# Optimization experiments

Measured on AMD Instinct MI355X. Metric: run time of the kernel, lower is better.

## Reference

```python
import jax, jax.numpy as jnp
import numpy as np
import math

B = 2
D = 256
NH, NL, NP = 8, 4, 4
DH = D // NH
DFF = 1024
NLAYERS = 6
SHAPES = [(96, 96), (48, 48), (24, 24), (12, 12)]
CINS = [256, 512, 768, 1024]
LQ = sum(h * w for h, w in SHAPES)


def setup_inputs() -> dict:
    key = jax.random.key(0)
    ks = iter(jax.random.split(key, 64))
    inp = {}
    for i, (cin, (h, w)) in enumerate(zip(CINS, SHAPES)):
        inp[f"x{i+1}"] = jax.random.normal(next(ks), (B, cin, h, w), jnp.float32)
        inp[f"fc{i+1}_w"] = jax.random.normal(next(ks), (D, cin), jnp.float32) / np.sqrt(cin)
        inp[f"fc{i+1}_b"] = jnp.zeros((D,), jnp.float32)
    inp["gn_g"] = jnp.ones((4, D), jnp.float32)
    inp["gn_b"] = jnp.zeros((4, D), jnp.float32)
    inp["level_embed"] = jax.random.normal(next(ks), (4, D), jnp.float32)
    def lin(k, o, i_, s=1.0):
        return jax.random.normal(k, (NLAYERS, o, i_), jnp.float32) * (s / np.sqrt(i_))
    inp["off_w"] = lin(next(ks), NH * NL * NP * 2, D, 0.01)  # small, like zero-init offsets
    inp["off_b"] = jax.random.normal(next(ks), (NLAYERS, NH * NL * NP * 2), jnp.float32) * 0.5
    inp["aw_w"] = lin(next(ks), NH * NL * NP, D)
    inp["aw_b"] = jnp.zeros((NLAYERS, NH * NL * NP), jnp.float32)
    inp["val_w"] = lin(next(ks), D, D)
    inp["val_b"] = jnp.zeros((NLAYERS, D), jnp.float32)
    inp["out_w"] = lin(next(ks), D, D)
    inp["out_b"] = jnp.zeros((NLAYERS, D), jnp.float32)
    inp["ln1_g"] = jnp.ones((NLAYERS, D), jnp.float32)
    inp["ln1_b"] = jnp.zeros((NLAYERS, D), jnp.float32)
    inp["l1_w"] = lin(next(ks), DFF, D)
    inp["l1_b"] = jnp.zeros((NLAYERS, DFF), jnp.float32)
    inp["l2_w"] = lin(next(ks), D, DFF)
    inp["l2_b"] = jnp.zeros((NLAYERS, D), jnp.float32)
    inp["ln2_g"] = jnp.ones((NLAYERS, D), jnp.float32)
    inp["ln2_b"] = jnp.zeros((NLAYERS, D), jnp.float32)
    return inp


def layer_norm(x, g, b, eps=1e-5):
    m = x.mean(-1, keepdims=True)
    v = ((x - m) ** 2).mean(-1, keepdims=True)
    return (x - m) / jnp.sqrt(v + eps) * g + b


def group_norm(x, g, b, groups=32, eps=1e-5):
    # x: [B, L, C]; torch GroupNorm applied on [B, C, L] -> normalize over (group-channels, L)
    Bq, L, C = x.shape
    xg = x.reshape(Bq, L, groups, C // groups)
    m = xg.mean(axis=(1, 3), keepdims=True)
    v = ((xg - m) ** 2).mean(axis=(1, 3), keepdims=True)
    xg = (xg - m) / jnp.sqrt(v + eps)
    return xg.reshape(Bq, L, C) * g + b


def sine_pos(Hl, Wl):
    # DETR PositionEmbeddingSine, normalize=True, mask all-zero -> cumsum = arange(1..)
    eps, scale, T, npf = 1e-6, 2 * math.pi, 10000.0, D // 2
    ye = (jnp.arange(1, Hl + 1, dtype=jnp.float32) / (Hl + eps)) * scale
    xe = (jnp.arange(1, Wl + 1, dtype=jnp.float32) / (Wl + eps)) * scale
    dim_t = T ** (2 * (jnp.arange(npf) // 2).astype(jnp.float32) / npf)
    def emb(e):
        p = e[:, None] / dim_t
        return jnp.stack([jnp.sin(p[:, 0::2]), jnp.cos(p[:, 1::2])], -1).reshape(-1, npf)
    py, px = emb(ye), emb(xe)
    pos = jnp.concatenate([
        jnp.broadcast_to(py[:, None, :], (Hl, Wl, npf)),
        jnp.broadcast_to(px[None, :, :], (Hl, Wl, npf))], -1)
    return pos.reshape(Hl * Wl, D)


def ref_points():
    # training path: all levels, valid_ratios == 1 (masks all zero)
    refs = []
    for (Hl, Wl) in SHAPES:
        ry = (jnp.arange(Hl, dtype=jnp.float32) + 0.5) / Hl
        rx = (jnp.arange(Wl, dtype=jnp.float32) + 0.5) / Wl
        gy, gx = jnp.meshgrid(ry, rx, indexing='ij')
        refs.append(jnp.stack([gx.ravel(), gy.ravel()], -1))
    r = jnp.concatenate(refs, 0)  # [LQ, 2]
    return jnp.broadcast_to(r[None, :, None, :], (B, LQ, NL, 2))


def ms_deform(value, locs, attw):
    # value: [B, Lin, NH, DH]; locs: [B, Lq, NH, NL, NP, 2] in [0,1]; attw: [B, Lq, NH, NL, NP]
    Bq, Lq = locs.shape[0], locs.shape[1]
    out = jnp.zeros((Bq, Lq, NH, DH), value.dtype)
    start = 0
    for l, (Hl, Wl) in enumerate(SHAPES):
        vf = value[:, start:start + Hl * Wl].transpose(0, 2, 1, 3)  # [B, NH, HW, DH]
        start += Hl * Wl
        loc = locs[:, :, :, l]  # [B, Lq, NH, NP, 2]
        # grid_sample align_corners=False unnormalize: (2u-1+1)/2*W - 0.5 = u*W - 0.5
        x = loc[..., 0] * Wl - 0.5
        y = loc[..., 1] * Hl - 0.5
        x0, y0 = jnp.floor(x), jnp.floor(y)
        tx, ty = x - x0, y - y0
        samp = jnp.zeros((Bq, NH, Lq * NP, DH), value.dtype)
        for dx, dy, w in ((0, 0, (1 - tx) * (1 - ty)), (1, 0, tx * (1 - ty)),
                          (0, 1, (1 - tx) * ty), (1, 1, tx * ty)):
            xi, yi = x0 + dx, y0 + dy
            valid = (xi >= 0) & (xi < Wl) & (yi >= 0) & (yi < Hl)  # zero padding
            idx = (jnp.clip(yi, 0, Hl - 1) * Wl + jnp.clip(xi, 0, Wl - 1)).astype(jnp.int32)
            idxr = idx.transpose(0, 2, 1, 3).reshape(Bq, NH, Lq * NP)
            g = jnp.take_along_axis(vf, idxr[..., None], axis=2)  # [B, NH, Lq*NP, DH]
            wr = (w * valid).transpose(0, 2, 1, 3).reshape(Bq, NH, Lq * NP, 1)
            samp = samp + g * wr
        samp = samp.reshape(Bq, NH, Lq, NP, DH)
        out = out + jnp.einsum('bnqpd,bqnp->bqnd', samp, attw[:, :, :, l])
    return out.reshape(Bq, Lq, NH * DH)


def enc_layer(src, pos, ref, p):
    q = src + pos
    Bq, Lq, _ = src.shape
    off = (q @ p['off_w'].T + p['off_b']).reshape(Bq, Lq, NH, NL, NP, 2)
    aw = jax.nn.softmax((q @ p['aw_w'].T + p['aw_b']).reshape(Bq, Lq, NH, NL * NP), -1)
    aw = aw.reshape(Bq, Lq, NH, NL, NP)
    val = (src @ p['val_w'].T + p['val_b']).reshape(Bq, Lq, NH, DH)
    norml = jnp.array([[w, h] for (h, w) in SHAPES], jnp.float32)  # [NL, 2] as (W, H)
    locs = ref[:, :, None, :, None, :] + off / norml[None, None, None, :, None, :]
    att = ms_deform(val, locs, aw) @ p['out_w'].T + p['out_b']
    src = layer_norm(src + att, p['ln1_g'], p['ln1_b'])
    h = jax.nn.relu(src @ p['l1_w'].T + p['l1_b'])
    src = layer_norm(src + h @ p['l2_w'].T + p['l2_b'], p['ln2_g'], p['ln2_b'])
    return src


LAYER_KEYS = ['off_w', 'off_b', 'aw_w', 'aw_b', 'val_w', 'val_b', 'out_w', 'out_b',
              'ln1_g', 'ln1_b', 'l1_w', 'l1_b', 'l2_w', 'l2_b', 'ln2_g', 'ln2_b']


def _forward(x1, x2, x3, x4, fcs, gn_g, gn_b, level_embed, stacks):
    xs = [x1, x2, x3, x4]
    toks, poss = [], []
    for i, x in enumerate(xs):
        Bq, c, h, w = x.shape
        f = x.reshape(Bq, c, h * w).transpose(0, 2, 1)  # b (h w) c
        t = group_norm(f @ fcs[i][0].T + fcs[i][1], gn_g[i], gn_b[i])
        toks.append(t)
        poss.append(jnp.broadcast_to((sine_pos(h, w) + level_embed[i])[None], (Bq, h * w, D)))
    src = jnp.concatenate(toks, 1)
    pos = jnp.concatenate(poss, 1)
    ref = ref_points()
    for l in range(NLAYERS):
        p = {k: stacks[k][l] for k in LAYER_KEYS}
        src = enc_layer(src, pos, ref, p)
    return src


def reference(x1, x2, x3, x4, fc1_w, fc1_b, fc2_w, fc2_b, fc3_w, fc3_b, fc4_w, fc4_b,
              gn_g, gn_b, level_embed, off_w, off_b, aw_w, aw_b, val_w, val_b, out_w, out_b,
              ln1_g, ln1_b, l1_w, l1_b, l2_w, l2_b, ln2_g, ln2_b):
    fcs = [(fc1_w, fc1_b), (fc2_w, fc2_b), (fc3_w, fc3_b), (fc4_w, fc4_b)]
    stacks = dict(off_w=off_w, off_b=off_b, aw_w=aw_w, aw_b=aw_b, val_w=val_w, val_b=val_b,
                  out_w=out_w, out_b=out_b, ln1_g=ln1_g, ln1_b=ln1_b, l1_w=l1_w, l1_b=l1_b,
                  l2_w=l2_w, l2_b=l2_b, ln2_g=ln2_g, ln2_b=ln2_b)
    src = _forward(x1, x2, x3, x4, fcs, gn_g, gn_b, level_embed, stacks)
    spatial_shapes = jnp.array(SHAPES, jnp.int32)
    level_start_index = jnp.concatenate([jnp.zeros((1,), jnp.int32),
                                         jnp.cumsum(spatial_shapes.prod(1))[:-1]])
    valid_ratios = jnp.ones((B, NL, 2), jnp.float32)
    return (src, level_start_index, spatial_shapes, valid_ratios)
```

## Files before the change

### kernel.cpp

```cpp
#include <hip/hip_runtime.h>
#include <math.h>

#define DD 256
#define DFFN 1024
#define LQT 12240
#define BB 2
#define MROWS (BB * LQT)

typedef __attribute__((ext_vector_type(8))) short short8v;
typedef __attribute__((ext_vector_type(4))) float floatx4;

__device__ __forceinline__ unsigned short f2bf(float x) {
    unsigned int u = __builtin_bit_cast(unsigned int, x);
    u = (u + 0x7fffu + ((u >> 16) & 1u)) >> 16;
    return (unsigned short)u;
}
__device__ __forceinline__ float bf2f(unsigned short h) {
    unsigned int u = ((unsigned int)h) << 16;
    return __builtin_bit_cast(float, u);
}

__device__ __forceinline__ void gload16(const unsigned short* g, unsigned short* lds) {
    __builtin_amdgcn_global_load_lds(
        (const __attribute__((address_space(1))) unsigned int*)g,
        (__attribute__((address_space(3))) unsigned int*)lds, 16, 0, 0);
}

__device__ __forceinline__ void level_of(int q, int& lvl, int& start, int& S) {
    if (q < 9216)       { lvl = 0; start = 0;     S = 96; }
    else if (q < 11520) { lvl = 1; start = 9216;  S = 48; }
    else if (q < 12096) { lvl = 2; start = 11520; S = 24; }
    else                { lvl = 3; start = 12096; S = 12; }
}

__global__ __launch_bounds__(256)
void gemm_qkv(const unsigned short* __restrict__ Aq,
              const unsigned short* __restrict__ Asr,
              const unsigned short* __restrict__ Woff,
              const unsigned short* __restrict__ Waw,
              const unsigned short* __restrict__ Wval,
              const float* __restrict__ boff, const float* __restrict__ baw,
              const float* __restrict__ bval,
              float* __restrict__ awbo, unsigned short* __restrict__ offo,
              unsigned short* __restrict__ valo)
{
    __shared__ alignas(16) unsigned short As[2][4][64][8];
    __shared__ alignas(16) unsigned short Bs[2][4][128][8];
    const int t = threadIdx.x;
    const int m0 = blockIdx.x * 64;
    const int y = blockIdx.y;
    const unsigned short* A; const unsigned short* Wb; const float* bi;
    int nb, mode;
    if (y < 3) {
        A = Aq;
        if (y < 2) { Wb = Woff; bi = boff; nb = y * 128; mode = 0; }
        else       { Wb = Waw;  bi = baw;  nb = 0;       mode = 1; }
    } else {
        A = Asr; Wb = Wval; bi = bval; nb = (y - 3) * 128; mode = 2;
    }
    const int wv = __builtin_amdgcn_readfirstlane(t >> 6);
    const int lane = t & 63;
    const int wm = wv >> 1, wn = wv & 1;
    const int kb = lane >> 4, lr = lane & 15;

    const int ar = min(m0 + lane, MROWS - 1);
    const unsigned short* gA  = A  + (long)ar * 256 + wv * 8;
    const unsigned short* gB0 = Wb + (long)(nb + lane) * 256 + wv * 8;
    const unsigned short* gB1 = Wb + (long)(nb + 64 + lane) * 256 + wv * 8;

    floatx4 acc[2][4];
    #pragma unroll
    for (int m = 0; m < 2; ++m)
        #pragma unroll
        for (int n = 0; n < 4; ++n)
            acc[m][n] = (floatx4){0.f, 0.f, 0.f, 0.f};

    gload16(gA,  &As[0][wv][0][0]);
    gload16(gB0, &Bs[0][wv][0][0]);
    gload16(gB1, &Bs[0][wv][64][0]);
    gA += 32; gB0 += 32; gB1 += 32;
    __syncthreads();

    #pragma unroll
    for (int kt = 0; kt < 8; ++kt) {
        const int cur = kt & 1;
        if (kt < 7) {
            gload16(gA,  &As[cur ^ 1][wv][0][0]);
            gload16(gB0, &Bs[cur ^ 1][wv][0][0]);
            gload16(gB1, &Bs[cur ^ 1][wv][64][0]);
            gA += 32; gB0 += 32; gB1 += 32;
        }
        short8v av[2], bv[4];
        #pragma unroll
        for (int m = 0; m < 2; ++m)
            av[m] = *(const short8v*)&As[cur][kb][wm * 32 + m * 16 + lr][0];
        #pragma unroll
        for (int n = 0; n < 4; ++n)
            bv[n] = *(const short8v*)&Bs[cur][kb][wn * 64 + n * 16 + lr][0];
        #pragma unroll
        for (int m = 0; m < 2; ++m)
            #pragma unroll
            for (int n = 0; n < 4; ++n)
                acc[m][n] = __builtin_amdgcn_mfma_f32_16x16x32_bf16(
                    av[m], bv[n], acc[m][n], 0, 0, 0);
        __syncthreads();
    }

    const int lh = lane >> 4;
    #pragma unroll
    for (int m = 0; m < 2; ++m) {
        const int row0 = m0 + wm * 32 + m * 16 + lh * 4;
        #pragma unroll
        for (int n = 0; n < 4; ++n) {
            const int col = nb + wn * 64 + n * 16 + lr;
            const float b = bi[col];
            #pragma unroll
            for (int r = 0; r < 4; ++r) {
                const int row = row0 + r;
                if (row >= MROWS) continue;
                const float v = acc[m][n][r] + b;
                if (mode == 0)      offo[(long)row * 256 + col] = f2bf(v);
                else if (mode == 1) awbo[(long)row * 128 + col] = v;
                else                valo[(long)row * 256 + col] = f2bf(v);
            }
        }
    }
}

__global__ __launch_bounds__(256)
void gemm64(const unsigned short* __restrict__ A, long aZ,
            const unsigned short* __restrict__ W,
            const float* __restrict__ bias,
            float* __restrict__ Cf, long cZ,
            int M, int N, int K)
{
    __shared__ alignas(16) unsigned short As[2][4][64][8];
    __shared__ alignas(16) unsigned short Bs[2][4][128][8];
    const int t = threadIdx.x;
    const int z = blockIdx.z;
    A  += (long)z * aZ;
    Cf += (long)z * cZ;
    const int m0 = blockIdx.x * 64;
    const int n0 = blockIdx.y * 128;
    const int wv = __builtin_amdgcn_readfirstlane(t >> 6);
    const int lane = t & 63;
    const int wm = wv >> 1, wn = wv & 1;
    const int kb = lane >> 4, lr = lane & 15;

    const int ar = min(m0 + lane, M - 1);
    const unsigned short* gA  = A + (long)ar * K + wv * 8;
    const unsigned short* gB0 = W + (long)(n0 + lane) * K + wv * 8;
    const unsigned short* gB1 = W + (long)(n0 + 64 + lane) * K + wv * 8;

    floatx4 acc[2][4];
    #pragma unroll
    for (int m = 0; m < 2; ++m)
        #pragma unroll
        for (int n = 0; n < 4; ++n)
            acc[m][n] = (floatx4){0.f, 0.f, 0.f, 0.f};

    gload16(gA,  &As[0][wv][0][0]);
    gload16(gB0, &Bs[0][wv][0][0]);
    gload16(gB1, &Bs[0][wv][64][0]);
    gA += 32; gB0 += 32; gB1 += 32;
    __syncthreads();

    const int nk = K >> 5;
    for (int kt = 0; kt < nk; ++kt) {
        const int cur = kt & 1;
        if (kt + 1 < nk) {
            gload16(gA,  &As[cur ^ 1][wv][0][0]);
            gload16(gB0, &Bs[cur ^ 1][wv][0][0]);
            gload16(gB1, &Bs[cur ^ 1][wv][64][0]);
            gA += 32; gB0 += 32; gB1 += 32;
        }
        short8v av[2], bv[4];
        #pragma unroll
        for (int m = 0; m < 2; ++m)
            av[m] = *(const short8v*)&As[cur][kb][wm * 32 + m * 16 + lr][0];
        #pragma unroll
        for (int n = 0; n < 4; ++n)
            bv[n] = *(const short8v*)&Bs[cur][kb][wn * 64 + n * 16 + lr][0];
        #pragma unroll
        for (int m = 0; m < 2; ++m)
            #pragma unroll
            for (int n = 0; n < 4; ++n)
                acc[m][n] = __builtin_amdgcn_mfma_f32_16x16x32_bf16(
                    av[m], bv[n], acc[m][n], 0, 0, 0);
        __syncthreads();
    }

    const int lh = lane >> 4;
    #pragma unroll
    for (int m = 0; m < 2; ++m) {
        const int row0 = m0 + wm * 32 + m * 16 + lh * 4;
        #pragma unroll
        for (int n = 0; n < 4; ++n) {
            const int col = n0 + wn * 64 + n * 16 + lr;
            const float b = bias[col];
            #pragma unroll
            for (int r = 0; r < 4; ++r) {
                const int row = row0 + r;
                if (row >= M) continue;
                Cf[(long)row * N + col] = acc[m][n][r] + b;
            }
        }
    }
}

__global__ __launch_bounds__(256)
void gemm128(const unsigned short* __restrict__ A,
             const unsigned short* __restrict__ W,
             const float* __restrict__ bias, unsigned short* __restrict__ Ch,
             int M, int N, int K)
{
    __shared__ alignas(16) unsigned short As[2][4][128][8];
    __shared__ alignas(16) unsigned short Bs[2][4][128][8];
    const int t = threadIdx.x;
    const int m0 = blockIdx.x * 128;
    const int n0 = blockIdx.y * 128;
    const int wv = __builtin_amdgcn_readfirstlane(t >> 6);
    const int lane = t & 63;
    const int wm = wv >> 1, wn = wv & 1;
    const int kb = lane >> 4, lr = lane & 15;

    const int r0 = min(m0 + lane, M - 1);
    const int r1 = min(m0 + 64 + lane, M - 1);
    const unsigned short* gA0 = A + (long)r0 * K + wv * 8;
    const unsigned short* gA1 = A + (long)r1 * K + wv * 8;
    const unsigned short* gB0 = W + (long)(n0 + lane) * K + wv * 8;
    const unsigned short* gB1 = W + (long)(n0 + 64 + lane) * K + wv * 8;

    floatx4 acc[4][4];
    #pragma unroll
    for (int m = 0; m < 4; ++m)
        #pragma unroll
        for (int n = 0; n < 4; ++n)
            acc[m][n] = (floatx4){0.f, 0.f, 0.f, 0.f};

    gload16(gA0, &As[0][wv][0][0]);
    gload16(gA1, &As[0][wv][64][0]);
    gload16(gB0, &Bs[0][wv][0][0]);
    gload16(gB1, &Bs[0][wv][64][0]);
    gA0 += 32; gA1 += 32; gB0 += 32; gB1 += 32;
    __syncthreads();

    const int nk = K >> 5;
    for (int kt = 0; kt < nk; ++kt) {
        const int cur = kt & 1;
        if (kt + 1 < nk) {
            gload16(gA0, &As[cur ^ 1][wv][0][0]);
            gload16(gA1, &As[cur ^ 1][wv][64][0]);
            gload16(gB0, &Bs[cur ^ 1][wv][0][0]);
            gload16(gB1, &Bs[cur ^ 1][wv][64][0]);
            gA0 += 32; gA1 += 32; gB0 += 32; gB1 += 32;
        }
        short8v av[4], bv[4];
        #pragma unroll
        for (int m = 0; m < 4; ++m)
            av[m] = *(const short8v*)&As[cur][kb][wm * 64 + m * 16 + lr][0];
        #pragma unroll
        for (int n = 0; n < 4; ++n)
            bv[n] = *(const short8v*)&Bs[cur][kb][wn * 64 + n * 16 + lr][0];
        #pragma unroll
        for (int m = 0; m < 4; ++m)
            #pragma unroll
            for (int n = 0; n < 4; ++n)
                acc[m][n] = __builtin_amdgcn_mfma_f32_16x16x32_bf16(
                    av[m], bv[n], acc[m][n], 0, 0, 0);
        __syncthreads();
    }

    const int lh = lane >> 4;
    #pragma unroll
    for (int m = 0; m < 4; ++m) {
        const int row0 = m0 + wm * 64 + m * 16 + lh * 4;
        #pragma unroll
        for (int n = 0; n < 4; ++n) {
            const int col = n0 + wn * 64 + n * 16 + lr;
            const float b = bias[col];
            #pragma unroll
            for (int r = 0; r < 4; ++r) {
                const int row = row0 + r;
                if (row >= M) continue;
                Ch[(long)row * N + col] = f2bf(fmaxf(acc[m][n][r] + b, 0.f));
            }
        }
    }
}

__global__ __launch_bounds__(256)
void gemm_ln(const unsigned short* __restrict__ A,
             const unsigned short* __restrict__ W,
             const float* __restrict__ bias, const unsigned short* R,
             const float* __restrict__ lg, const float* __restrict__ lb,
             float* outf, unsigned short* outh,
             const float* __restrict__ pos, unsigned short* __restrict__ qout,
             int M, int K)
{
    __shared__ alignas(16) unsigned short As[2][4][32][8];
    __shared__ alignas(16) unsigned short Bs[2][4][256][8];
    __shared__ float red[32][4][2];
    __shared__ float smean[32], sinv[32];
    const int t = threadIdx.x;
    const int m0 = blockIdx.x * 32;
    const int wv = __builtin_amdgcn_readfirstlane(t >> 6);
    const int lane = t & 63;
    const int kb = lane >> 4, lr = lane & 15;
    const int lh = kb;

    const unsigned short* gA = A + (long)(m0 + (lane & 31)) * K
                                 + (wv * 2 + (lane >> 5)) * 8;
    const unsigned short* gB0 = W + (long)lane * K + wv * 8;
    const unsigned short* gB1 = W + (long)(64 + lane) * K + wv * 8;
    const unsigned short* gB2 = W + (long)(128 + lane) * K + wv * 8;
    const unsigned short* gB3 = W + (long)(192 + lane) * K + wv * 8;

    floatx4 acc[2][4];
    #pragma unroll
    for (int m = 0; m < 2; ++m)
        #pragma unroll
        for (int n = 0; n < 4; ++n)
            acc[m][n] = (floatx4){0.f, 0.f, 0.f, 0.f};

    if (wv < 2) gload16(gA, &As[0][wv * 2][0][0]);
    gload16(gB0, &Bs[0][wv][0][0]);
    gload16(gB1, &Bs[0][wv][64][0]);
    gload16(gB2, &Bs[0][wv][128][0]);
    gload16(gB3, &Bs[0][wv][192][0]);
    gA += 32; gB0 += 32; gB1 += 32; gB2 += 32; gB3 += 32;
    __syncthreads();

    const int nk = K >> 5;
    for (int kt = 0; kt < nk; ++kt) {
        const int cur = kt & 1;
        if (kt + 1 < nk) {
            if (wv < 2) gload16(gA, &As[cur ^ 1][wv * 2][0][0]);
            gload16(gB0, &Bs[cur ^ 1][wv][0][0]);
            gload16(gB1, &Bs[cur ^ 1][wv][64][0]);
            gload16(gB2, &Bs[cur ^ 1][wv][128][0]);
            gload16(gB3, &Bs[cur ^ 1][wv][192][0]);
            gA += 32; gB0 += 32; gB1 += 32; gB2 += 32; gB3 += 32;
        }
        short8v av[2], bv[4];
        #pragma unroll
        for (int m = 0; m < 2; ++m)
            av[m] = *(const short8v*)&As[cur][kb][m * 16 + lr][0];
        #pragma unroll
        for (int n = 0; n < 4; ++n)
            bv[n] = *(const short8v*)&Bs[cur][kb][wv * 64 + n * 16 + lr][0];
        #pragma unroll
        for (int m = 0; m < 2; ++m)
            #pragma unroll
            for (int n = 0; n < 4; ++n)
                acc[m][n] = __builtin_amdgcn_mfma_f32_16x16x32_bf16(
                    av[m], bv[n], acc[m][n], 0, 0, 0);
        __syncthreads();
    }

    #pragma unroll
    for (int n = 0; n < 4; ++n) {
        const int col = wv * 64 + n * 16 + lr;
        const float bcol = bias[col];
        #pragma unroll
        for (int m = 0; m < 2; ++m) {
            #pragma unroll
            for (int r = 0; r < 4; ++r) {
                const int grow = m0 + m * 16 + lh * 4 + r;
                acc[m][n][r] += bcol + bf2f(R[(long)grow * 256 + col]);
            }
        }
    }
    #pragma unroll
    for (int m = 0; m < 2; ++m) {
        #pragma unroll
        for (int r = 0; r < 4; ++r) {
            float s = acc[m][0][r] + acc[m][1][r] + acc[m][2][r] + acc[m][3][r];
            float q = acc[m][0][r] * acc[m][0][r] + acc[m][1][r] * acc[m][1][r]
                    + acc[m][2][r] * acc[m][2][r] + acc[m][3][r] * acc[m][3][r];
            #pragma unroll
            for (int o = 1; o < 16; o <<= 1) {
                s += __shfl_xor(s, o);
                q += __shfl_xor(q, o);
            }
            if (lr == 0) {
                red[m * 16 + lh * 4 + r][wv][0] = s;
                red[m * 16 + lh * 4 + r][wv][1] = q;
            }
        }
    }
    __syncthreads();
    if (t < 32) {
        const float s = red[t][0][0] + red[t][1][0] + red[t][2][0] + red[t][3][0];
        const float q = red[t][0][1] + red[t][1][1] + red[t][2][1] + red[t][3][1];
        const float mean = s * (1.f / 256.f);
        smean[t] = mean;
        sinv[t] = rsqrtf(q * (1.f / 256.f) - mean * mean + 1e-5f);
    }
    __syncthreads();
    #pragma unroll
    for (int n = 0; n < 4; ++n) {
        const int col = wv * 64 + n * 16 + lr;
        const float gc = lg[col], bc = lb[col];
        #pragma unroll
        for (int m = 0; m < 2; ++m) {
            #pragma unroll
            for (int r = 0; r < 4; ++r) {
                const int row = m * 16 + lh * 4 + r;
                const int grow = m0 + row;
                const float y = (acc[m][n][r] - smean[row]) * sinv[row] * gc + bc;
                const long o = (long)grow * 256 + col;
                outh[o] = f2bf(y);
                if (outf) outf[o] = y;
                if (qout) {
                    const int qrow = grow - (grow >= LQT ? LQT : 0);
                    qout[o] = f2bf(y + pos[(long)qrow * 256 + col]);
                }
            }
        }
    }
}

__global__ __launch_bounds__(256)
void tp_k(const float* __restrict__ x, unsigned short* __restrict__ xt,
          int C, int Ml)
{
    __shared__ float tile[32][33];
    const int m0 = blockIdx.x * 32, c0 = blockIdx.y * 32;
    const int zb = blockIdx.z;
    const float* px = x + (long)zb * C * Ml;
    unsigned short* pxt = xt + (long)zb * Ml * C;
    const int t = threadIdx.x;
    {
        const int cl = t >> 3, m4 = (t & 7) * 4;
        const int gm = m0 + m4;
        if (gm < Ml) {
            const float4 v = *(const float4*)(px + (long)(c0 + cl) * Ml + gm);
            tile[cl][m4 + 0] = v.x; tile[cl][m4 + 1] = v.y;
            tile[cl][m4 + 2] = v.z; tile[cl][m4 + 3] = v.w;
        }
    }
    __syncthreads();
    {
        const int ml = t >> 3, c4 = (t & 7) * 4;
        const int gm = m0 + ml;
        if (gm < Ml) {
            ushort4 o;
            o.x = f2bf(tile[c4 + 0][ml]);
            o.y = f2bf(tile[c4 + 1][ml]);
            o.z = f2bf(tile[c4 + 2][ml]);
            o.w = f2bf(tile[c4 + 3][ml]);
            *(ushort4*)(pxt + (long)gm * C + c0 + c4) = o;
        }
    }
}

__global__ __launch_bounds__(256)
void gn_part(const float* __restrict__ src, float* __restrict__ part)
{
    const int x = blockIdx.x;
    const int b = x >> 7, c = x & 127;
    int lvl, chunk;
    if (c < 96)       { lvl = 0; chunk = c; }
    else if (c < 120) { lvl = 1; chunk = c - 96; }
    else if (c < 126) { lvl = 2; chunk = c - 120; }
    else              { lvl = 3; chunk = c - 126; }
    const int starts[4] = {0, 9216, 11520, 12096};
    const int crows[4]  = {96, 96, 96, 72};
    const int rows = crows[lvl];
    const long base = ((long)b * LQT + starts[lvl] + (long)chunk * rows) * DD;
    const int t = threadIdx.x;
    float s = 0.f, sq = 0.f;
    for (int r = 0; r < rows; ++r) {
        const float v = src[base + (long)r * DD + t];
        s += v; sq += v * v;
    }
    #pragma unroll
    for (int o = 1; o < 8; o <<= 1) {
        s  += __shfl_xor(s, o);
        sq += __shfl_xor(sq, o);
    }
    if ((t & 7) == 0) {
        float* p = part + ((long)x * 32 + (t >> 3)) * 2;
        p[0] = s; p[1] = sq;
    }
}

__global__ void gn_fin(const float* __restrict__ part, float* __restrict__ stat)
{
    const int t = threadIdx.x;
    const int b = t >> 7, rest = t & 127;
    const int lvl = rest >> 5, grp = rest & 31;
    const int cbase[4] = {0, 96, 120, 126};
    const int ccnt[4]  = {96, 24, 6, 2};
    const int Ml[4]    = {9216, 2304, 576, 144};
    float s = 0.f, sq = 0.f;
    for (int i = 0; i < ccnt[lvl]; ++i) {
        const float* p = part + ((long)(b * 128 + cbase[lvl] + i) * 32 + grp) * 2;
        s += p[0]; sq += p[1];
    }
// ... 195 lines not shown
                              hipStream_t stream)
{
    const float* xs[4]  = {(const float*)d_in[0], (const float*)d_in[3],
                           (const float*)d_in[6], (const float*)d_in[9]};
    const float* fcw[4] = {(const float*)d_in[1], (const float*)d_in[4],
                           (const float*)d_in[7], (const float*)d_in[10]};
    const float* fcb[4] = {(const float*)d_in[2], (const float*)d_in[5],
                           (const float*)d_in[8], (const float*)d_in[11]};
    const float* gn_g = (const float*)d_in[12];
    const float* gn_b = (const float*)d_in[13];
    const float* lemb = (const float*)d_in[14];
    const float* off_w = (const float*)d_in[15];
    const float* off_b = (const float*)d_in[16];
    const float* aw_w  = (const float*)d_in[17];
    const float* aw_b  = (const float*)d_in[18];
    const float* val_w = (const float*)d_in[19];
    const float* val_b = (const float*)d_in[20];
    const float* out_w = (const float*)d_in[21];
    const float* out_b = (const float*)d_in[22];
    const float* ln1_g = (const float*)d_in[23];
    const float* ln1_b = (const float*)d_in[24];
    const float* l1_w  = (const float*)d_in[25];
    const float* l1_b  = (const float*)d_in[26];
    const float* l2_w  = (const float*)d_in[27];
    const float* l2_b  = (const float*)d_in[28];
    const float* ln2_g = (const float*)d_in[29];
    const float* ln2_b = (const float*)d_in[30];

    float* src = (float*)d_out;
    float* ws = (float*)d_ws;
    float* pos = ws;
    float* awb = pos + 3133440;
    unsigned short* bigbuf = (unsigned short*)(awb + 3133440);
    unsigned short* xt     = bigbuf;
    unsigned short* off_bf = bigbuf;
    unsigned short* val_bf = bigbuf + 6266880;
    unsigned short* msd_bf = bigbuf + 12533760;
    unsigned short* hid_bf = bigbuf;
    unsigned short* q_bf   = bigbuf + 25067520;
    unsigned short* src_bf = q_bf + 6266880;
    unsigned short* wb     = src_bf + 6266880;
    unsigned short* wb_fc[4];
    wb_fc[0] = wb;
    wb_fc[1] = wb_fc[0] + 65536;
    wb_fc[2] = wb_fc[1] + 131072;
    wb_fc[3] = wb_fc[2] + 196608;
    unsigned short* wb_off = wb_fc[3] + 262144;
    unsigned short* wb_aw  = wb_off + 393216;
    unsigned short* wb_val = wb_aw  + 196608;
    unsigned short* wb_out = wb_val + 393216;
    unsigned short* wb_l1  = wb_out + 393216;
    unsigned short* wb_l2  = wb_l1  + 1572864;
    float* part = (float*)(wb_l2 + 1572864);
    float* stat = part + 16384;
    (void)in_sizes; (void)n_in; (void)out_size; (void)ws_size;

    const int CINS[4]   = {256, 512, 768, 1024};
    const int SS[4]     = {96, 48, 24, 12};
    const int STARTS[4] = {0, 9216, 11520, 12096};
    const long XTOFF[4] = {0, 4718592, 7077888, 7962624};

    pos_k<<<LQT, 256, 0, stream>>>(pos, lemb);
    wcvt_k<<<(WCVT_TOTAL / 4 + 255) / 256, 256, 0, stream>>>(
        fcw[0], fcw[1], fcw[2], fcw[3], off_w, aw_w, val_w, out_w, l1_w, l2_w, wb);

    for (int i = 0; i < 4; ++i) {
        const int Ml = SS[i] * SS[i];
        tp_k<<<dim3((Ml + 31) / 32, CINS[i] / 32, BB), 256, 0, stream>>>(
            xs[i], xt + XTOFF[i], CINS[i], Ml);
    }
    for (int i = 0; i < 4; ++i) {
        const int Ml = SS[i] * SS[i];
        gemm64<<<dim3((Ml + 63) / 64, 2, BB), 256, 0, stream>>>(
            xt + XTOFF[i], (long)Ml * CINS[i],
            wb_fc[i], fcb[i],
            src + (long)STARTS[i] * DD, (long)LQT * DD,
            Ml, DD, CINS[i]);
    }
    gn_part<<<256, 256, 0, stream>>>(src, part);
    gn_fin<<<1, 256, 0, stream>>>(part, stat);
    gn_apply<<<MROWS / 4, 256, 0, stream>>>(src, src_bf, q_bf, stat, gn_g, gn_b, pos);

    for (int l = 0; l < 6; ++l) {
        gemm_qkv<<<dim3(383, 5), 256, 0, stream>>>(
            q_bf, src_bf,
            wb_off + (long)l * 65536, wb_aw + (long)l * 32768,
            wb_val + (long)l * 65536,
            off_b + l * DD, aw_b + l * 128, val_b + l * DD,
            awb, off_bf, val_bf);
        msdeform_k<<<MROWS / 2, 256, 0, stream>>>(val_bf, off_bf, awb, msd_bf);
        gemm_ln<<<765, 256, 0, stream>>>(
            msd_bf, wb_out + (long)l * 65536, out_b + l * DD, src_bf,
            ln1_g + l * DD, ln1_b + l * DD, nullptr, src_bf,
            nullptr, nullptr, MROWS, DD);
        gemm128<<<dim3(192, 8), 256, 0, stream>>>(
            src_bf, wb_l1 + (long)l * 262144, l1_b + l * DFFN, hid_bf,
            MROWS, DFFN, DD);
        const bool last = (l == 5);
        gemm_ln<<<765, 256, 0, stream>>>(
            hid_bf, wb_l2 + (long)l * 262144, l2_b + l * DD, src_bf,
            ln2_g + l * DD, ln2_b + l * DD, last ? src : nullptr, src_bf,
            last ? nullptr : pos, last ? nullptr : q_bf, MROWS, DFFN);
    }
    tail_k<<<1, 32, 0, stream>>>(src + (long)BB * LQT * DD);
}
```

Measured before the change: 1.593 ms.

## Stage whole A tile in LDS once and stream weights from global to registers

After: 1.731 ms. +8.7%, slower.

```diff
diff --git a/kernel.cpp b/kernel.cpp
--- a/kernel.cpp
+++ b/kernel.cpp
@@ -33,95 +33,255 @@
     else                { lvl = 3; start = 12096; S = 12; }
 }
 
-__global__ __launch_bounds__(256)
-void gemm_qkv(const unsigned short* __restrict__ Aq,
-              const unsigned short* __restrict__ Asr,
-              const unsigned short* __restrict__ Woff,
-              const unsigned short* __restrict__ Waw,
-              const unsigned short* __restrict__ Wval,
-              const float* __restrict__ boff, const float* __restrict__ baw,
-              const float* __restrict__ bval,
-              float* __restrict__ awbo, unsigned short* __restrict__ offo,
-              unsigned short* __restrict__ valo)
-{
-    __shared__ alignas(16) unsigned short As[2][4][64][8];
-    __shared__ alignas(16) unsigned short Bs[2][4][128][8];
-    const int t = threadIdx.x;
+template<int MF, int NF, int KO>
+__device__ __forceinline__ void as_core(const unsigned short* __restrict__ A,
+                                        const unsigned short* __restrict__ W,
+                                        unsigned short* AsD, int m0, int ncol0,
+                                        int M, floatx4 (&acc)[MF][NF])
+{
+    constexpr int BM = MF * 16;
+    constexpr int K  = KO * 32;
+    const int t = threadIdx.x;
+    const int wv = t >> 6, lane = t & 63;
+    const int lr = lane & 15;
+
+    constexpr int CH = BM * K / 512;
+    constexpr int PW = CH / 4;
+    #pragma unroll
+    for (int c = 0; c < PW; ++c) {
+        const int ch = wv * PW + c;
+        int row, sl;
+        if (BM == 64) { row = lane;      sl = ch; }
+        else          { row = lane & 31; sl = 2 * ch + (lane >> 5); }
+        gload16(A + (long)min(m0 + row, M - 1) * K + sl * 8, AsD + ch * 512);
+    }
+    __syncthreads();
+
+    const unsigned short* bp[NF];
+    #pragma unroll
+    for (int nf = 0; nf < NF; ++nf)
+        bp[nf] = W + (long)(ncol0 + nf * 16 + lr) * K + (lane >> 4) * 8;
+    const unsigned short* ap = AsD + (lane >> 4) * BM * 8 + lr * 8;
+
+    uint4 b0[NF], b1[NF];
+    short8v a0[MF], a1[MF];
+    #pragma unroll
+    for (int nf = 0; nf < NF; ++nf) b0[nf] = *(const uint4*)(bp[nf]);
+    #pragma unroll
+    for (int m = 0; m < MF; ++m)   a0[m] = *(const short8v*)(ap + m * 128);
+
+    for (int ko = 0; ko < KO; ko += 2) {
+        #pragma unroll
+        for (int nf = 0; nf < NF; ++nf)
+            b1[nf] = *(const uint4*)(bp[nf] + (ko + 1) * 32);
+        #pragma unroll
+        for (int m = 0; m < MF; ++m)
+            a1[m] = *(const short8v*)(ap + (long)(ko + 1) * BM * 32 + m * 128);
+        #pragma unroll
+        for (int m = 0; m < MF; ++m)
+            #pragma unroll
+            for (int nf = 0; nf < NF; ++nf)
+                acc[m][nf] = __builtin_amdgcn_mfma_f32_16x16x32_bf16(
+                    a0[m], __builtin_bit_cast(short8v, b0[nf]), acc[m][nf], 0, 0, 0);
+        if (ko + 2 < KO) {
+            #pragma unroll
+            for (int nf = 0; nf < NF; ++nf)
+                b0[nf] = *(const uint4*)(bp[nf] + (ko + 2) * 32);
+            #pragma unroll
+            for (int m = 0; m < MF; ++m)
+                a0[m] = *(const short8v*)(ap + (long)(ko + 2) * BM * 32 + m * 128);
+        }
+        #pragma unroll
+        for (int m = 0; m < MF; ++m)
+            #pragma unroll
+            for (int nf = 0; nf < NF; ++nf)
+                acc[m][nf] = __builtin_amdgcn_mfma_f32_16x16x32_bf16(
+                    a1[m], __builtin_bit_cast(short8v, b1[nf]), acc[m][nf], 0, 0, 0);
+    }
+}
+
+__global__ __launch_bounds__(256)
+void gemm_as_qkv(const unsigned short* __restrict__ Aq,
+                 const unsigned short* __restrict__ Asr,
+                 const unsigned short* __restrict__ Woff,
+                 const unsigned short* __restrict__ Waw,
+                 const unsigned short* __restrict__ Wval,
+                 const float* __restrict__ boff, const float* __restrict__ baw,
+                 const float* __restrict__ bval,
+                 float* __restrict__ awbo, unsigned short* __restrict__ offo,
+                 unsigned short* __restrict__ valo, int M)
+{
+    extern __shared__ __align__(16) unsigned short AsD[];
+    const int y = blockIdx.y;
     const int m0 = blockIdx.x * 64;
-    const int y = blockIdx.y;
-    const unsigned short* A; const unsigned short* Wb; const float* bi;
+    const unsigned short* A; const unsigned short* W; const float* bi;
     int nb, mode;
     if (y < 3) {
         A = Aq;
-        if (y < 2) { Wb = Woff; bi = boff; nb = y * 128; mode = 0; }
-        else       { Wb = Waw;  bi = baw;  nb = 0;       mode = 1; }
+        if (y < 2) { W = Woff; bi = boff; nb = y * 128; mode = 0; }
+        else       { W = Waw;  bi = baw;  nb = 0;       mode = 1; }
     } else {
-        A = Asr; Wb = Wval; bi = bval; nb = (y - 3) * 128; mode = 2;
-    }
-    const int wv = __builtin_amdgcn_readfirstlane(t >> 6);
-    const int lane = t & 63;
-    const int wm = wv >> 1, wn = wv & 1;
-    const int kb = lane >> 4, lr = lane & 15;
-
-    const int ar = min(m0 + lane, MROWS - 1);
-    const unsigned short* gA  = A  + (long)ar * 256 + wv * 8;
-    const unsigned short* gB0 = Wb + (long)(nb + lane) * 256 + wv * 8;
-    const unsigned short* gB1 = Wb + (long)(nb + 64 + lane) * 256 + wv * 8;
-
-    floatx4 acc[2][4];
-    #pragma unroll
-    for (int m = 0; m < 2; ++m)
-        #pragma unroll
-        for (int n = 0; n < 4; ++n)
+        A = Asr; W = Wval; bi = bval; nb = (y - 3) * 128; mode = 2;
+    }
+    const int t = threadIdx.x;
+    const int wv = t >> 6, lane = t & 63, lr = lane & 15, lh = lane >> 4;
+
+    floatx4 acc[4][2];
+    #pragma unroll
+    for (int m = 0; m < 4; ++m)
+        #pragma unroll
+        for (int n = 0; n < 2; ++n)
             acc[m][n] = (floatx4){0.f, 0.f, 0.f, 0.f};
 
-    gload16(gA,  &As[0][wv][0][0]);
-    gload16(gB0, &Bs[0][wv][0][0]);
-    gload16(gB1, &Bs[0][wv][64][0]);
-    gA += 32; gB0 += 32; gB1 += 32;
-    __syncthreads();
-
-    #pragma unroll
-    for (int kt = 0; kt < 8; ++kt) {
-        const int cur = kt & 1;
-        if (kt < 7) {
-            gload16(gA,  &As[cur ^ 1][wv][0][0]);
-            gload16(gB0, &Bs[cur ^ 1][wv][0][0]);
-            gload16(gB1, &Bs[cur ^ 1][wv][64][0]);
-            gA += 32; gB0 += 32; gB1 += 32;
-        }
-        short8v av[2], bv[4];
-        #pragma unroll
-        for (int m = 0; m < 2; ++m)
-            av[m] = *(const short8v*)&As[cur][kb][wm * 32 + m * 16 + lr][0];
-        #pragma unroll
-        for (int n = 0; n < 4; ++n)
-            bv[n] = *(const short8v*)&Bs[cur][kb][wn * 64 + n * 16 + lr][0];
-        #pragma unroll
-        for (int m = 0; m < 2; ++m)
-            #pragma unroll
-            for (int n = 0; n < 4; ++n)
-                acc[m][n] = __builtin_amdgcn_mfma_f32_16x16x32_bf16(
-                    av[m], bv[n], acc[m][n], 0, 0, 0);
-        __syncthreads();
-    }
-
-    const int lh = lane >> 4;
-    #pragma unroll
-    for (int m = 0; m < 2; ++m) {
-        const int row0 = m0 + wm * 32 + m * 16 + lh * 4;
-        #pragma unroll
-        for (int n = 0; n < 4; ++n) {
-            const int col = nb + wn * 64 + n * 16 + lr;
+    as_core<4, 2, 8>(A, W, AsD, m0, nb + wv * 32, M, acc);
+
+    #pragma unroll
+    for (int m = 0; m < 4; ++m) {
+        #pragma unroll
+        for (int nf = 0; nf < 2; ++nf) {
+            const int col = nb + wv * 32 + nf * 16 + lr;
             const float b = bi[col];
             #pragma unroll
             for (int r = 0; r < 4; ++r) {
-                const int row = row0 + r;
-                if (row >= MROWS) continue;
-                const float v = acc[m][n][r] + b;
+                const int row = m0 + m * 16 + lh * 4 + r;
+                if (row >= M) continue;
+                const float v = acc[m][nf][r] + b;
                 if (mode == 0)      offo[(long)row * 256 + col] = f2bf(v);
                 else if (mode == 1) awbo[(long)row * 128 + col] = v;
                 else                valo[(long)row * 256 + col] = f2bf(v);
+            }
+        }
+    }
+}
+
+__global__ __launch_bounds__(256)
+void gemm_as_relu(const unsigned short* __restrict__ A,
+                  const unsigned short* __restrict__ W,
+                  const float* __restrict__ bias,
+                  unsigned short* __restrict__ Ch, int M)
+{
+    extern __shared__ __align__(16) unsigned short AsD[];
+    const int m0 = blockIdx.x * 64;
+    const int n0 = blockIdx.y * 256;
+    const int t = threadIdx.x;
+    const int wv = t >> 6, lane = t & 63, lr = lane & 15, lh = lane >> 4;
+
+    floatx4 acc[4][4];
+    #pragma unroll
+    for (int m = 0; m < 4; ++m)
+        #pragma unroll
+        for (int n = 0; n < 4; ++n)
+            acc[m][n] = (floatx4){0.f, 0.f, 0.f, 0.f};
+
+    as_core<4, 4, 8>(A, W, AsD, m0, n0 + wv * 64, M, acc);
+
+    #pragma unroll
+    for (int m = 0; m < 4; ++m) {
+        #pragma unroll
+        for (int nf = 0; nf < 4; ++nf) {
+            const int col = n0 + wv * 64 + nf * 16 + lr;
+            const float b = bias[col];
+            #pragma unroll
+            for (int r = 0; r < 4; ++r) {
+                const int row = m0 + m * 16 + lh * 4 + r;
+                if (row >= M) continue;
+                Ch[(long)row * 1024 + col] = f2bf(fmaxf(acc[m][nf][r] + b, 0.f));
+            }
+        }
+    }
+}
+
+template<int MF, int KO>
+__global__ __launch_bounds__(256)
+void gemm_as_ln(const unsigned short* __restrict__ A,
+                const unsigned short* __restrict__ W,
+                const float* __restrict__ bias, const unsigned short* R,
+                const float* __restrict__ lg, const float* __restrict__ lb,
+                float* outf, unsigned short* outh,
+                const float* __restrict__ pos, unsigned short* __restrict__ qout,
+                int M)
+{
+    extern __shared__ __align__(16) unsigned short AsD[];
+    constexpr int BM = MF * 16;
+    const int m0 = blockIdx.x * BM;
+    const int t = threadIdx.x;
+    const int wv = t >> 6, lane = t & 63, lr = lane & 15, lh = lane >> 4;
+
+    floatx4 acc[MF][4];
+    #pragma unroll
+    for (int m = 0; m < MF; ++m)
+        #pragma unroll
+        for (int n = 0; n < 4; ++n)
+            acc[m][n] = (floatx4){0.f, 0.f, 0.f, 0.f};
+
+    as_core<MF, 4, KO>(A, W, AsD, m0, wv * 64, M, acc);
+
+    __syncthreads();
+    float* red   = (float*)AsD;
+    float* smean = red + BM * 8;
+    float* sinv  = smean + BM;
+
+    #pragma unroll
+    for (int nf = 0; nf < 4; ++nf) {
+        const int col = wv * 64 + nf * 16 + lr;
+        const float bcol = bias[col];
+        #pragma unroll
+        for (int m = 0; m < MF; ++m) {
+            #pragma unroll
+            for (int r = 0; r < 4; ++r) {
+                const int grow = m0 + m * 16 + lh * 4 + r;
+                const int rr = min(grow, M - 1);
+                acc[m][nf][r] += bcol + bf2f(R[(long)rr * 256 + col]);
+            }
+        }
+    }
+    #pragma unroll
+    for (int m = 0; m < MF; ++m) {
+        #pragma unroll
+        for (int r = 0; r < 4; ++r) {
+            float s = acc[m][0][r] + acc[m][1][r] + acc[m][2][r] + acc[m][3][r];
+            float q = acc[m][0][r] * acc[m][0][r] + acc[m][1][r] * acc[m][1][r]
+                    + acc[m][2][r] * acc[m][2][r] + acc[m][3][r] * acc[m][3][r];
+            #pragma unroll
+            for (int o = 1; o < 16; o <<= 1) {
+                s += __shfl_xor(s, o);
+                q += __shfl_xor(q, o);
+            }
+            if (lr == 0) {
+                const int row = m * 16 + lh * 4 + r;
+                red[row * 8 + wv * 2 + 0] = s;
+                red[row * 8 + wv * 2 + 1] = q;
+            }
+        }
+    }
+    __syncthreads();
+    if (t < BM) {
+        const float s = red[t * 8 + 0] + red[t * 8 + 2] + red[t * 8 + 4] + red[t * 8 + 6];
+        const float q = red[t * 8 + 1] + red[t * 8 + 3] + red[t * 8 + 5] + red[t * 8 + 7];
+        const float mean = s * (1.f / 256.f);
+        smean[t] = mean;
+        sinv[t] = rsqrtf(q * (1.f / 256.f) - mean * mean + 1e-5f);
+    }
+    __syncthreads();
+    #pragma unroll
+    for (int nf = 0; nf < 4; ++nf) {
+        const int col = wv * 64 + nf * 16 + lr;
+        const float gc = lg[col], bc = lb[col];
+        #pragma unroll
+        for (int m = 0; m < MF; ++m) {
+            #pragma unroll
+            for (int r = 0; r < 4; ++r) {
+                const int row = m * 16 + lh * 4 + r;
+                const int grow = m0 + row;
+                if (grow >= M) continue;
+                const float y = (acc[m][nf][r] - smean[row]) * sinv[row] * gc + bc;
+                const long o = (long)grow * 256 + col;
+                outh[o] = f2bf(y);
+                if (outf) outf[o] = y;
+                if (qout) {
+                    const int qrow = grow - (grow >= LQT ? LQT : 0);
+                    qout[o] = f2bf(y + pos[(long)qrow * 256 + col]);
+                }
             }
         }
     }
@@ -203,219 +363,6 @@
                 const int row = row0 + r;
                 if (row >= M) continue;
                 Cf[(long)row * N + col] = acc[m][n][r] + b;
-            }
-        }
-    }
-}
-
-__global__ __launch_bounds__(256)
-void gemm128(const unsigned short* __restrict__ A,
-             const unsigned short* __restrict__ W,
-             const float* __restrict__ bias, unsigned short* __restrict__ Ch,
-             int M, int N, int K)
-{
-    __shared__ alignas(16) unsigned short As[2][4][128][8];
-    __shared__ alignas(16) unsigned short Bs[2][4][128][8];
-    const int t = threadIdx.x;
-    const int m0 = blockIdx.x * 128;
-    const int n0 = blockIdx.y * 128;
-    const int wv = __builtin_amdgcn_readfirstlane(t >> 6);
-    const int lane = t & 63;
-    const int wm = wv >> 1, wn = wv & 1;
-    const int kb = lane >> 4, lr = lane & 15;
-
-    const int r0 = min(m0 + lane, M - 1);
-    const int r1 = min(m0 + 64 + lane, M - 1);
-    const unsigned short* gA0 = A + (long)r0 * K + wv * 8;
-    const unsigned short* gA1 = A + (long)r1 * K + wv * 8;
-    const unsigned short* gB0 = W + (long)(n0 + lane) * K + wv * 8;
-    const unsigned short* gB1 = W + (long)(n0 + 64 + lane) * K + wv * 8;
-
-    floatx4 acc[4][4];
-    #pragma unroll
-    for (int m = 0; m < 4; ++m)
-        #pragma unroll
-        for (int n = 0; n < 4; ++n)
-            acc[m][n] = (floatx4){0.f, 0.f, 0.f, 0.f};
-
-    gload16(gA0, &As[0][wv][0][0]);
-    gload16(gA1, &As[0][wv][64][0]);
-    gload16(gB0, &Bs[0][wv][0][0]);
-    gload16(gB1, &Bs[0][wv][64][0]);
-    gA0 += 32; gA1 += 32; gB0 += 32; gB1 += 32;
-    __syncthreads();
-
-    const int nk = K >> 5;
-    for (int kt = 0; kt < nk; ++kt) {
-        const int cur = kt & 1;
-        if (kt + 1 < nk) {
-            gload16(gA0, &As[cur ^ 1][wv][0][0]);
-            gload16(gA1, &As[cur ^ 1][wv][64][0]);
-            gload16(gB0, &Bs[cur ^ 1][wv][0][0]);
-            gload16(gB1, &Bs[cur ^ 1][wv][64][0]);
-            gA0 += 32; gA1 += 32; gB0 += 32; gB1 += 32;
-        }
-        short8v av[4], bv[4];
-        #pragma unroll
-        for (int m = 0; m < 4; ++m)
-            av[m] = *(const short8v*)&As[cur][kb][wm * 64 + m * 16 + lr][0];
-        #pragma unroll
-        for (int n = 0; n < 4; ++n)
-            bv[n] = *(const short8v*)&Bs[cur][kb][wn * 64 + n * 16 + lr][0];
-        #pragma unroll
-        for (int m = 0; m < 4; ++m)
-            #pragma unroll
-            for (int n = 0; n < 4; ++n)
-                acc[m][n] = __builtin_amdgcn_mfma_f32_16x16x32_bf16(
-                    av[m], bv[n], acc[m][n], 0, 0, 0);
-        __syncthreads();
-    }
-
-    const int lh = lane >> 4;
-    #pragma unroll
-    for (int m = 0; m < 4; ++m) {
-        const int row0 = m0 + wm * 64 + m * 16 + lh * 4;
-        #pragma unroll
-        for (int n = 0; n < 4; ++n) {
-            const int col = n0 + wn * 64 + n * 16 + lr;
-            const float b = bias[col];
-            #pragma unroll
-            for (int r = 0; r < 4; ++r) {
-                const int row = row0 + r;
-                if (row >= M) continue;
-                Ch[(long)row * N + col] = f2bf(fmaxf(acc[m][n][r] + b, 0.f));
-            }
-        }
-    }
-}
-
-__global__ __launch_bounds__(256)
-void gemm_ln(const unsigned short* __restrict__ A,
-             const unsigned short* __restrict__ W,
-             const float* __restrict__ bias, const unsigned short* R,
-             const float* __restrict__ lg, const float* __restrict__ lb,
-             float* outf, unsigned short* outh,
-             const float* __restrict__ pos, unsigned short* __restrict__ qout,
-             int M, int K)
-{
-    __shared__ alignas(16) unsigned short As[2][4][32][8];
-    __shared__ alignas(16) unsigned short Bs[2][4][256][8];
-    __shared__ float red[32][4][2];
-    __shared__ float smean[32], sinv[32];
-    const int t = threadIdx.x;
-    const int m0 = blockIdx.x * 32;
-    const int wv = __builtin_amdgcn_readfirstlane(t >> 6);
-    const int lane = t & 63;
-    const int kb = lane >> 4, lr = lane & 15;
-    const int lh = kb;
-
-    const unsigned short* gA = A + (long)(m0 + (lane & 31)) * K
-                                 + (wv * 2 + (lane >> 5)) * 8;
-    const unsigned short* gB0 = W + (long)lane * K + wv * 8;
-    const unsigned short* gB1 = W + (long)(64 + lane) * K + wv * 8;
-    const unsigned short* gB2 = W + (long)(128 + lane) * K + wv * 8;
-    const unsigned short* gB3 = W + (long)(192 + lane) * K + wv * 8;
-
-    floatx4 acc[2][4];
-    #pragma unroll
-    for (int m = 0; m < 2; ++m)
-        #pragma unroll
-        for (int n = 0; n < 4; ++n)
-            acc[m][n] = (floatx4){0.f, 0.f, 0.f, 0.f};
-
-    if (wv < 2) gload16(gA, &As[0][wv * 2][0][0]);
-    gload16(gB0, &Bs[0][wv][0][0]);
-    gload16(gB1, &Bs[0][wv][64][0]);
-    gload16(gB2, &Bs[0][wv][128][0]);
-    gload16(gB3, &Bs[0][wv][192][0]);
-    gA += 32; gB0 += 32; gB1 += 32; gB2 += 32; gB3 += 32;
-    __syncthreads();
-
-    const int nk = K >> 5;
-    for (int kt = 0; kt < nk; ++kt) {
-        const int cur = kt & 1;
-        if (kt + 1 < nk) {
-            if (wv < 2) gload16(gA, &As[cur ^ 1][wv * 2][0][0]);
-            gload16(gB0, &Bs[cur ^ 1][wv][0][0]);
-            gload16(gB1, &Bs[cur ^ 1][wv][64][0]);
-            gload16(gB2, &Bs[cur ^ 1][wv][128][0]);
-            gload16(gB3, &Bs[cur ^ 1][wv][192][0]);
-            gA += 32; gB0 += 32; gB1 += 32; gB2 += 32; gB3 += 32;
-        }
-        short8v av[2], bv[4];
-        #pragma unroll
-        for (int m = 0; m < 2; ++m)
-            av[m] = *(const short8v*)&As[cur][kb][m * 16 + lr][0];
-        #pragma unroll
-        for (int n = 0; n < 4; ++n)
-            bv[n] = *(const short8v*)&Bs[cur][kb][wv * 64 + n * 16 + lr][0];
-        #pragma unroll
-        for (int m = 0; m < 2; ++m)
-            #pragma unroll
-            for (int n = 0; n < 4; ++n)
-                acc[m][n] = __builtin_amdgcn_mfma_f32_16x16x32_bf16(
-                    av[m], bv[n], acc[m][n], 0, 0, 0);
-        __syncthreads();
-    }
-
-    #pragma unroll
-    for (int n = 0; n < 4; ++n) {
-        const int col = wv * 64 + n * 16 + lr;
-        const float bcol = bias[col];
-        #pragma unroll
-        for (int m = 0; m < 2; ++m) {
-            #pragma unroll
-            for (int r = 0; r < 4; ++r) {
-                const int grow = m0 + m * 16 + lh * 4 + r;
-                acc[m][n][r] += bcol + bf2f(R[(long)grow * 256 + col]);
-            }
-        }
-    }
-    #pragma unroll
-    for (int m = 0; m < 2; ++m) {
-        #pragma unroll
-        for (int r = 0; r < 4; ++r) {
-            float s = acc[m][0][r] + acc[m][1][r] + acc[m][2][r] + acc[m][3][r];
-            float q = acc[m][0][r] * acc[m][0][r] + acc[m][1][r] * acc[m][1][r]
-                    + acc[m][2][r] * acc[m][2][r] + acc[m][3][r] * acc[m][3][r];
-            #pragma unroll
-            for (int o = 1; o < 16; o <<= 1) {
-                s += __shfl_xor(s, o);
-                q += __shfl_xor(q, o);
-            }
-            if (lr == 0) {
-                red[m * 16 + lh * 4 + r][wv][0] = s;
-                red[m * 16 + lh * 4 + r][wv][1] = q;
-            }
-        }
-    }
-    __syncthreads();
-    if (t < 32) {
-        const float s = red[t][0][0] + red[t][1][0] + red[t][2][0] + red[t][3][0];
-        const float q = red[t][0][1] + red[t][1][1] + red[t][2][1] + red[t][3][1];
-        const float mean = s * (1.f / 256.f);
-        smean[t] = mean;
-        sinv[t] = rsqrtf(q * (1.f / 256.f) - mean * mean + 1e-5f);
-    }
-    __syncthreads();
-    #pragma unroll
-    for (int n = 0; n < 4; ++n) {
-        const int col = wv * 64 + n * 16 + lr;
-        const float gc = lg[col], bc = lb[col];
-        #pragma unroll
-        for (int m = 0; m < 2; ++m) {
-            #pragma unroll
-            for (int r = 0; r < 4; ++r) {
-                const int row = m * 16 + lh * 4 + r;
-                const int grow = m0 + row;
-                const float y = (acc[m][n][r] - smean[row]) * sinv[row] * gc + bc;
-                const long o = (long)grow * 256 + col;
-                outh[o] = f2bf(y);
-                if (outf) outf[o] = y;
-                if (qout) {
-                    const int qrow = grow - (grow >= LQT ? LQT : 0);
-                    qout[o] = f2bf(y + pos[(long)qrow * 256 + col]);
-                }
             }
         }
     }
@@ -777,25 +724,24 @@
     gn_apply<<<MROWS / 4, 256, 0, stream>>>(src, src_bf, q_bf, stat, gn_g, gn_b, pos);
 
     for (int l = 0; l < 6; ++l) {
-        gemm_qkv<<<dim3(383, 5), 256, 0, stream>>>(
+        gemm_as_qkv<<<dim3(383, 5), 256, 32768, stream>>>(
             q_bf, src_bf,
             wb_off + (long)l * 65536, wb_aw + (long)l * 32768,
             wb_val + (long)l * 65536,
             off_b + l * DD, aw_b + l * 128, val_b + l * DD,
-            awb, off_bf, val_bf);
+            awb, off_bf, val_bf, MROWS);
         msdeform_k<<<MROWS / 2, 256, 0, stream>>>(val_bf, off_bf, awb, msd_bf);
-        gemm_ln<<<765, 256, 0, stream>>>(
+        gemm_as_ln<4, 8><<<383, 256, 32768, stream>>>(
             msd_bf, wb_out + (long)l * 65536, out_b + l * DD, src_bf,
             ln1_g + l * DD, ln1_b + l * DD, nullptr, src_bf,
-            nullptr, nullptr, MROWS, DD);
-        gemm128<<<dim3(192, 8), 256, 0, stream>>>(
-            src_bf, wb_l1 + (long)l * 262144, l1_b + l * DFFN, hid_bf,
-            MROWS, DFFN, DD);
+            nullptr, nullptr, MROWS);
+        gemm_as_relu<<<dim3(383, 4), 256, 32768, stream>>>(
+            src_bf, wb_l1 + (long)l * 262144, l1_b + l * DFFN, hid_bf, MROWS);
         const bool last = (l == 5);
-        gemm_ln<<<765, 256, 0, stream>>>(
+        gemm_as_ln<2, 32><<<765, 256, 65536, stream>>>(
             hid_bf, wb_l2 + (long)l * 262144, l2_b + l * DD, src_bf,
             ln2_g + l * DD, ln2_b + l * DD, last ? src : nullptr, src_bf,
-            last ? nullptr : pos, last ? nullptr : q_bf, MROWS, DFFN);
+            last ? nullptr : pos, last ? nullptr : q_bf, MROWS);
     }
     tail_k<<<1, 32, 0, stream>>>(src + (long)BB * LQT * DD);
 }
```

## Triple-buffer GEMM LDS tiles with one barrier per k-step and explicit vmcnt waits

Applied to the files above, without the earlier changes.

Result: slower. 1.803 ms (+13.2%).

```diff
diff --git a/kernel.cpp b/kernel.cpp
--- a/kernel.cpp
+++ b/kernel.cpp
@@ -9,6 +9,9 @@
 
 typedef __attribute__((ext_vector_type(8))) short short8v;
 typedef __attribute__((ext_vector_type(4))) float floatx4;
+
+#define VMW(N) asm volatile("s_waitcnt vmcnt(" #N ")" ::: "memory")
+#define SBAR() asm volatile("s_barrier" ::: "memory")
 
 __device__ __forceinline__ unsigned short f2bf(float x) {
     unsigned int u = __builtin_bit_cast(unsigned int, x);
@@ -44,8 +47,8 @@
               float* __restrict__ awbo, unsigned short* __restrict__ offo,
               unsigned short* __restrict__ valo)
 {
-    __shared__ alignas(16) unsigned short As[2][4][64][8];
-    __shared__ alignas(16) unsigned short Bs[2][4][128][8];
+    __shared__ alignas(16) unsigned short As[3][4][64][8];
+    __shared__ alignas(16) unsigned short Bs[3][4][128][8];
     const int t = threadIdx.x;
     const int m0 = blockIdx.x * 64;
     const int y = blockIdx.y;
@@ -75,21 +78,23 @@
         for (int n = 0; n < 4; ++n)
             acc[m][n] = (floatx4){0.f, 0.f, 0.f, 0.f};
 
-    gload16(gA,  &As[0][wv][0][0]);
-    gload16(gB0, &Bs[0][wv][0][0]);
-    gload16(gB1, &Bs[0][wv][64][0]);
-    gA += 32; gB0 += 32; gB1 += 32;
-    __syncthreads();
-
-    #pragma unroll
+    gload16(gA,       &As[0][wv][0][0]);
+    gload16(gB0,      &Bs[0][wv][0][0]);
+    gload16(gB1,      &Bs[0][wv][64][0]);
+    gload16(gA  + 32, &As[1][wv][0][0]);
+    gload16(gB0 + 32, &Bs[1][wv][0][0]);
+    gload16(gB1 + 32, &Bs[1][wv][64][0]);
+
     for (int kt = 0; kt < 8; ++kt) {
-        const int cur = kt & 1;
-        if (kt < 7) {
-            gload16(gA,  &As[cur ^ 1][wv][0][0]);
-            gload16(gB0, &Bs[cur ^ 1][wv][0][0]);
-            gload16(gB1, &Bs[cur ^ 1][wv][64][0]);
-            gA += 32; gB0 += 32; gB1 += 32;
-        }
+        if (kt < 7) VMW(3); else VMW(0);
+        SBAR();
+        if (kt + 2 < 8) {
+            const int nb3 = (kt + 2) % 3;
+            gload16(gA  + (kt + 2) * 32, &As[nb3][wv][0][0]);
+            gload16(gB0 + (kt + 2) * 32, &Bs[nb3][wv][0][0]);
+            gload16(gB1 + (kt + 2) * 32, &Bs[nb3][wv][64][0]);
+        }
+        const int cur = kt % 3;
         short8v av[2], bv[4];
         #pragma unroll
         for (int m = 0; m < 2; ++m)
@@ -103,7 +108,6 @@
             for (int n = 0; n < 4; ++n)
                 acc[m][n] = __builtin_amdgcn_mfma_f32_16x16x32_bf16(
                     av[m], bv[n], acc[m][n], 0, 0, 0);
-        __syncthreads();
     }
 
     const int lh = lane >> 4;
@@ -214,8 +218,8 @@
              const float* __restrict__ bias, unsigned short* __restrict__ Ch,
              int M, int N, int K)
 {
-    __shared__ alignas(16) unsigned short As[2][4][128][8];
-    __shared__ alignas(16) unsigned short Bs[2][4][128][8];
+    __shared__ alignas(16) unsigned short As[3][4][128][8];
+    __shared__ alignas(16) unsigned short Bs[3][4][128][8];
     const int t = threadIdx.x;
     const int m0 = blockIdx.x * 128;
     const int n0 = blockIdx.y * 128;
@@ -238,23 +242,27 @@
         for (int n = 0; n < 4; ++n)
             acc[m][n] = (floatx4){0.f, 0.f, 0.f, 0.f};
 
-    gload16(gA0, &As[0][wv][0][0]);
-    gload16(gA1, &As[0][wv][64][0]);
-    gload16(gB0, &Bs[0][wv][0][0]);
-    gload16(gB1, &Bs[0][wv][64][0]);
-    gA0 += 32; gA1 += 32; gB0 += 32; gB1 += 32;
-    __syncthreads();
+    gload16(gA0,      &As[0][wv][0][0]);
+    gload16(gA1,      &As[0][wv][64][0]);
+    gload16(gB0,      &Bs[0][wv][0][0]);
+    gload16(gB1,      &Bs[0][wv][64][0]);
+    gload16(gA0 + 32, &As[1][wv][0][0]);
+    gload16(gA1 + 32, &As[1][wv][64][0]);
+    gload16(gB0 + 32, &Bs[1][wv][0][0]);
+    gload16(gB1 + 32, &Bs[1][wv][64][0]);
 
     const int nk = K >> 5;
     for (int kt = 0; kt < nk; ++kt) {
-        const int cur = kt & 1;
-        if (kt + 1 < nk) {
-            gload16(gA0, &As[cur ^ 1][wv][0][0]);
-            gload16(gA1, &As[cur ^ 1][wv][64][0]);
-            gload16(gB0, &Bs[cur ^ 1][wv][0][0]);
-            gload16(gB1, &Bs[cur ^ 1][wv][64][0]);
-            gA0 += 32; gA1 += 32; gB0 += 32; gB1 += 32;
-        }
+        if (kt < nk - 1) VMW(4); else VMW(0);
+        SBAR();
+        if (kt + 2 < nk) {
+            const int nb3 = (kt + 2) % 3;
+            gload16(gA0 + (kt + 2) * 32, &As[nb3][wv][0][0]);
+            gload16(gA1 + (kt + 2) * 32, &As[nb3][wv][64][0]);
+            gload16(gB0 + (kt + 2) * 32, &Bs[nb3][wv][0][0]);
+            gload16(gB1 + (kt + 2) * 32, &Bs[nb3][wv][64][0]);
+        }
+        const int cur = kt % 3;
         short8v av[4], bv[4];
         #pragma unroll
         for (int m = 0; m < 4; ++m)
@@ -268,7 +276,6 @@
             for (int n = 0; n < 4; ++n)
                 acc[m][n] = __builtin_amdgcn_mfma_f32_16x16x32_bf16(
                     av[m], bv[n], acc[m][n], 0, 0, 0);
-        __syncthreads();
     }
 
     const int lh = lane >> 4;
@@ -298,8 +305,8 @@
              const float* __restrict__ pos, unsigned short* __restrict__ qout,
              int M, int K)
 {
-    __shared__ alignas(16) unsigned short As[2][4][32][8];
-    __shared__ alignas(16) unsigned short Bs[2][4][256][8];
+    __shared__ alignas(16) unsigned short As[3][4][32][8];
+    __shared__ alignas(16) unsigned short Bs[3][4][256][8];
     __shared__ float red[32][4][2];
     __shared__ float smean[32], sinv[32];
     const int t = threadIdx.x;
@@ -328,20 +335,30 @@
     gload16(gB1, &Bs[0][wv][64][0]);
     gload16(gB2, &Bs[0][wv][128][0]);
     gload16(gB3, &Bs[0][wv][192][0]);
-    gA += 32; gB0 += 32; gB1 += 32; gB2 += 32; gB3 += 32;
-    __syncthreads();
+    if (wv < 2) gload16(gA + 32, &As[1][wv * 2][0][0]);
+    gload16(gB0 + 32, &Bs[1][wv][0][0]);
+    gload16(gB1 + 32, &Bs[1][wv][64][0]);
+    gload16(gB2 + 32, &Bs[1][wv][128][0]);
+    gload16(gB3 + 32, &Bs[1][wv][192][0]);
 
     const int nk = K >> 5;
     for (int kt = 0; kt < nk; ++kt) {
-        const int cur = kt & 1;
-        if (kt + 1 < nk) {
-            if (wv < 2) gload16(gA, &As[cur ^ 1][wv * 2][0][0]);
-            gload16(gB0, &Bs[cur ^ 1][wv][0][0]);
-            gload16(gB1, &Bs[cur ^ 1][wv][64][0]);
-            gload16(gB2, &Bs[cur ^ 1][wv][128][0]);
-            gload16(gB3, &Bs[cur ^ 1][wv][192][0]);
-            gA += 32; gB0 += 32; gB1 += 32; gB2 += 32; gB3 += 32;
-        }
+        if (kt < nk - 1) {
+            if (wv < 2) VMW(5); else VMW(4);
+        } else {
+            VMW(0);
+        }
+        SBAR();
+        if (kt + 2 < nk) {
+            const int nb3 = (kt + 2) % 3;
+            const int ko = (kt + 2) * 32;
+            if (wv < 2) gload16(gA + ko, &As[nb3][wv * 2][0][0]);
+            gload16(gB0 + ko, &Bs[nb3][wv][0][0]);
+            gload16(gB1 + ko, &Bs[nb3][wv][64][0]);
+            gload16(gB2 + ko, &Bs[nb3][wv][128][0]);
+            gload16(gB3 + ko, &Bs[nb3][wv][192][0]);
+        }
+        const int cur = kt % 3;
         short8v av[2], bv[4];
         #pragma unroll
         for (int m = 0; m < 2; ++m)
@@ -355,7 +372,6 @@
             for (int n = 0; n < 4; ++n)
                 acc[m][n] = __builtin_amdgcn_mfma_f32_16x16x32_bf16(
                     av[m], bv[n], acc[m][n], 0, 0, 0);
-        __syncthreads();
     }
 
     #pragma unroll
```
